# Kernel optimization log

Hardware: AMD Instinct MI355X
Metric: run time of the kernel (lower is better)

The kernel has to match this reference:

```python
import jax, jax.numpy as jnp
import numpy as np

MAX_SHIFT = 16

def setup_inputs() -> dict:
    key = jax.random.key(0)
    k1, k2 = jax.random.split(key)
    x = jax.random.normal(k1, (64, 3, 512, 512), dtype=jnp.float32)
    # emulate torch: normal(0, sigma=max_shift/2) -> int -> clamp(-max_shift, max_shift)
    shifts = jax.random.randint(k2, (64, 2), -MAX_SHIFT, MAX_SHIFT + 1, dtype=jnp.int32)
    return {"x": x, "shifts": shifts}

def reference(x, shifts):
    # x: [B, C, H, W]; shifts: [B, 2] circular shifts applied to dims (H, W)
    def roll_one(img, s):
        # img: [C, H, W]; roll dims 1 and 2 (H, W), matching torch dims=(1,2)
        return jnp.roll(img, (s[0], s[1]), axis=(1, 2))
    return jax.vmap(roll_one)(x, shifts)
```

## Files before the change

### kernel.cpp

```cpp
#include <hip/hip_runtime.h>

#define BATCH 64
#define CHAN  3
#define HH    512
#define WW    512
#define W4    (WW / 4)

__global__ __launch_bounds__(256) void roll_lds_kernel(
    const float4* __restrict__ x,
    const int*    __restrict__ shifts,
    float4*       __restrict__ out)
{
    __shared__ float4 lds[2 * W4];

    const int tid    = threadIdx.x;
    const int r      = tid >> 7;
    const int w4     = tid & (W4 - 1);
    const int row_id = blockIdx.x * 2 + r;
    const int bc     = row_id >> 9;
    const int h      = row_id & (HH - 1);
    const int b      = bc / CHAN;

    const int s0 = shifts[2 * b];
    const int s1 = shifts[2 * b + 1];

    const int hs = (h - s0) & (HH - 1);
    lds[tid] = x[((size_t)bc * HH + hs) * W4 + w4];
    __syncthreads();

    const int d  = (-s1) & (WW - 1);
    const int qd = d >> 2;
    const int rd = d & 3;
    const int qa = (w4 + qd) & (W4 - 1);
    const int qb = (qa + 1) & (W4 - 1);
    const float4 A = lds[(r << 7) + qa];
    const float4 B = lds[(r << 7) + qb];

    float4 o;
    if      (rd == 0) o = A;
    else if (rd == 1) o = make_float4(A.y, A.z, A.w, B.x);
    else if (rd == 2) o = make_float4(A.z, A.w, B.x, B.y);
    else              o = make_float4(A.w, B.x, B.y, B.z);

    out[row_id * W4 + w4] = o;
}

extern "C" void kernel_launch(void* const* d_in, const int* in_sizes, int n_in,
                              void* d_out, int out_size, void* d_ws, size_t ws_size,
                              hipStream_t stream)
{
    const float4* x      = (const float4*)d_in[0];
    const int*    shifts = (const int*)d_in[1];
    float4*       out    = (float4*)d_out;

    const int rows  = BATCH * CHAN * HH;
    const int grid  = rows / 2;
    const int block = 256;

    roll_lds_kernel<<<grid, block, 0, stream>>>(x, shifts, out);
}
```

Before: 319.4 us.

## Replace LDS staging with direct overlapping global loads and nontemporal stores

Drops the shared-memory staging and barrier. Each thread now reads its two neighbouring float4s straight from global memory, and the second read is expected to hit cache. Each block now handles 8 rows with 4 unrolled rows per thread to add memory-level parallelism, and output writes use nontemporal stores to avoid polluting cache. The cost is twice as many global load instructions, with lower block count and no LDS synchronization.

```diff
diff --git a/kernel.cpp b/kernel.cpp
--- a/kernel.cpp
+++ b/kernel.cpp
@@ -5,44 +5,56 @@
 #define HH    512
 #define WW    512
 #define W4    (WW / 4)
+#define ROWS_PER_BLOCK 8
 
-__global__ __launch_bounds__(256) void roll_lds_kernel(
+typedef float vfloat4 __attribute__((ext_vector_type(4)));
+
+__global__ __launch_bounds__(256) void roll_direct_kernel(
     const float4* __restrict__ x,
     const int*    __restrict__ shifts,
     float4*       __restrict__ out)
 {
-    __shared__ float4 lds[2 * W4];
-
-    const int tid    = threadIdx.x;
-    const int r      = tid >> 7;
-    const int w4     = tid & (W4 - 1);
-    const int row_id = blockIdx.x * 2 + r;
-    const int bc     = row_id >> 9;
-    const int h      = row_id & (HH - 1);
-    const int b      = bc / CHAN;
+    const int tid  = threadIdx.x;
+    const int w4   = tid & (W4 - 1);
+    const int rr   = tid >> 7;
+    const int row0 = blockIdx.x * ROWS_PER_BLOCK;
+    const int bc   = row0 >> 9;
+    const int h0   = row0 & (HH - 1);
+    const int b    = bc / CHAN;
 
     const int s0 = shifts[2 * b];
     const int s1 = shifts[2 * b + 1];
-
-    const int hs = (h - s0) & (HH - 1);
-    lds[tid] = x[((size_t)bc * HH + hs) * W4 + w4];
-    __syncthreads();
-
     const int d  = (-s1) & (WW - 1);
     const int qd = d >> 2;
     const int rd = d & 3;
     const int qa = (w4 + qd) & (W4 - 1);
     const int qb = (qa + 1) & (W4 - 1);
-    const float4 A = lds[(r << 7) + qa];
-    const float4 B = lds[(r << 7) + qb];
 
-    float4 o;
-    if      (rd == 0) o = A;
-    else if (rd == 1) o = make_float4(A.y, A.z, A.w, B.x);
-    else if (rd == 2) o = make_float4(A.z, A.w, B.x, B.y);
-    else              o = make_float4(A.w, B.x, B.y, B.z);
+    const float4* __restrict__ xb = x + (size_t)bc * HH * W4;
+    float4* __restrict__ ob = out + (size_t)row0 * W4 + w4;
 
-    out[row_id * W4 + w4] = o;
+    float4 A[4], Bq[4];
+    #pragma unroll
+    for (int i = 0; i < 4; ++i) {
+        const int h  = h0 + rr + 2 * i;
+        const int hs = (h - s0) & (HH - 1);
+        const float4* __restrict__ src = xb + (size_t)hs * W4;
+        A[i]  = src[qa];
+        Bq[i] = src[qb];
+    }
+
+    #pragma unroll
+    for (int i = 0; i < 4; ++i) {
+        const float4 a = A[i];
+        const float4 q = Bq[i];
+        float4 o;
+        if      (rd == 0) o = a;
+        else if (rd == 1) o = make_float4(a.y, a.z, a.w, q.x);
+        else if (rd == 2) o = make_float4(a.z, a.w, q.x, q.y);
+        else              o = make_float4(a.w, q.x, q.y, q.z);
+        vfloat4* dst = reinterpret_cast<vfloat4*>(&ob[(size_t)(rr + 2 * i) * W4]);
+        __builtin_nontemporal_store(__builtin_bit_cast(vfloat4, o), dst);
+    }
 }
 
 extern "C" void kernel_launch(void* const* d_in, const int* in_sizes, int n_in,
@@ -54,8 +66,8 @@
     float4*       out    = (float4*)d_out;
 
     const int rows  = BATCH * CHAN * HH;
-    const int grid  = rows / 2;
+    const int grid  = rows / ROWS_PER_BLOCK;
     const int block = 256;
 
-    roll_lds_kernel<<<grid, block, 0, stream>>>(x, shifts, out);
+    roll_direct_kernel<<<grid, block, 0, stream>>>(x, shifts, out);
 }
```

After: 336.9 us. 5.5% more time.
